# Kernel optimization log

Hardware: AMD Instinct MI355X
Metric: run time of the kernel (lower is better)

## Reference

```python
import jax
import jax.numpy as jnp
import numpy as np

NV, NH, COND_DIM, HW = 256, 256, 16, 64
B = 8192
T_END = 1.0
T_START = 5.0
FALLOFF = 0.1


def setup_inputs() -> dict:
    key = jax.random.key(0)
    ks = jax.random.split(key, 4)
    return {
        "cond": jax.random.normal(ks[0], (B, COND_DIM), dtype=jnp.float32),
        "W": jax.random.normal(ks[1], (NV, NH), dtype=jnp.float32) * 0.01,
        "b": jnp.zeros((NV,), jnp.float32),
        "c": jnp.zeros((NH,), jnp.float32),
        "fc1_w": jax.random.normal(ks[2], (HW, COND_DIM), dtype=jnp.float32) * (1.0 / np.sqrt(COND_DIM)),
        "fc1_b": jnp.zeros((HW,), jnp.float32),
        "fc2_w": jax.random.normal(ks[3], (2 * (NV + NH), HW), dtype=jnp.float32) * (1.0 / np.sqrt(HW)),
        "fc2_b": jnp.zeros((2 * (NV + NH),), jnp.float32),
        "steps": 32,
    }


def reference(cond, W, b, c, fc1_w, fc1_b, fc2_w, fc2_b, steps):
    nv, nh = W.shape
    # Conditioner: torch Linear convention y = x @ W.T + b
    x = jnp.tanh(cond @ fc1_w.T + fc1_b)
    x = x @ fc2_w.T + fc2_b  # [B, 2*(nv+nh)]
    gamma_b, beta_b, gamma_c, beta_c = jnp.split(x, [nv, 2 * nv, 2 * nv + nh], axis=-1)
    b_mod = (1.0 + gamma_b) * b + beta_b  # [B, nv]
    c_mod = (1.0 + gamma_c) * c + beta_c  # [B, nh]

    batch = cond.shape[0]
    key = jax.random.key(42)
    key, k0 = jax.random.split(key)
    v = jax.random.bernoulli(k0, 0.5, (batch, nv)).astype(W.dtype)
    s0 = jnp.ones((batch, 1), W.dtype)

    # sigmoid annealing schedule
    t = jnp.arange(steps, dtype=W.dtype)
    s = 1.0 / (1.0 + jnp.exp(FALLOFF * (t - steps / 2.0)))
    temps = T_END + (T_START - T_END) * s  # [steps]

    bsum = jnp.sum(b_mod, axis=-1)  # [B], constant across steps

    def gibbs_step(carry, T):
        v, s0, key = carry
        key, kh, ks0, kv = jax.random.split(key, 4)
        # symmetric flip of visibles
        v_eff = s0 * v + (1.0 - s0) * (1.0 - v)
        p_h = jax.nn.sigmoid((v_eff @ W + c_mod) / T)
        h = jax.random.bernoulli(kh, p_h).astype(v.dtype)  # [B, nh]
        a = h @ W.T  # [B, nv]
        vb = jnp.sum(v * b_mod, axis=-1)
        va = jnp.sum(v * a, axis=-1)
        asum = jnp.sum(a, axis=-1)
        dE = -bsum - asum + 2.0 * vb + 2.0 * va  # [B]
        p_s0 = jax.nn.sigmoid(dE / T)
        s0 = jax.random.bernoulli(ks0, p_s0).astype(v.dtype)[:, None]  # [B,1]
        p_v = jax.nn.sigmoid((a + b_mod) / T)
        v_eff2 = jax.random.bernoulli(kv, p_v).astype(v.dtype)
        v_next = s0 * v_eff2 + (1.0 - s0) * (1.0 - v_eff2)
        return (v_next, s0, key), None

    (v, s0, key), _ = jax.lax.scan(gibbs_step, (v, s0, key), temps)
    return v, temps
```

## Files before the change

kernel.cpp:

```cpp
#include <hip/hip_runtime.h>
#include <math.h>

#pragma clang fp contract(off)

namespace {

constexpr int kSteps = 32;

constexpr size_t OFF_TEMPS = 0;
constexpr size_t OFF_KEYS  = 64;
constexpr size_t OFF_WP    = 512;
constexpr size_t OFF_WTP   = 66048;
constexpr size_t OFF_F2T   = 131584;
constexpr size_t OFF_X1    = 197120;
constexpr size_t OFF_BMOD  = 721408;
constexpr size_t OFF_CMOD  = 2818560;
constexpr size_t WS_FLOATS = 4915712;

__device__ __forceinline__ unsigned rotl32(unsigned v, int n) {
  return (v << n) | (v >> (32 - n));
}

__device__ __forceinline__ void tf_block(unsigned k0, unsigned k1,
                                         unsigned c0, unsigned c1,
                                         unsigned* o0, unsigned* o1) {
  unsigned k2 = k0 ^ k1 ^ 0x1BD11BDAu;
  unsigned x0 = c0 + k0;
  unsigned x1 = c1 + k1;
  x0 += x1; x1 = rotl32(x1, 13); x1 ^= x0;
  x0 += x1; x1 = rotl32(x1, 15); x1 ^= x0;
  x0 += x1; x1 = rotl32(x1, 26); x1 ^= x0;
  x0 += x1; x1 = rotl32(x1, 6);  x1 ^= x0;
  x0 += k1; x1 += k2 + 1u;
  x0 += x1; x1 = rotl32(x1, 17); x1 ^= x0;
  x0 += x1; x1 = rotl32(x1, 29); x1 ^= x0;
  x0 += x1; x1 = rotl32(x1, 16); x1 ^= x0;
  x0 += x1; x1 = rotl32(x1, 24); x1 ^= x0;
  x0 += k2; x1 += k0 + 2u;
  x0 += x1; x1 = rotl32(x1, 13); x1 ^= x0;
  x0 += x1; x1 = rotl32(x1, 15); x1 ^= x0;
  x0 += x1; x1 = rotl32(x1, 26); x1 ^= x0;
  x0 += x1; x1 = rotl32(x1, 6);  x1 ^= x0;
  x0 += k0; x1 += k1 + 3u;
  x0 += x1; x1 = rotl32(x1, 17); x1 ^= x0;
  x0 += x1; x1 = rotl32(x1, 29); x1 ^= x0;
  x0 += x1; x1 = rotl32(x1, 16); x1 ^= x0;
  x0 += x1; x1 = rotl32(x1, 24); x1 ^= x0;
  x0 += k1; x1 += k2 + 4u;
  x0 += x1; x1 = rotl32(x1, 13); x1 ^= x0;
  x0 += x1; x1 = rotl32(x1, 15); x1 ^= x0;
  x0 += x1; x1 = rotl32(x1, 26); x1 ^= x0;
  x0 += x1; x1 = rotl32(x1, 6);  x1 ^= x0;
  x0 += k2; x1 += k0 + 5u;
  *o0 = x0; *o1 = x1;
}

__device__ __forceinline__ float tf_uniform(unsigned k0, unsigned k1, unsigned idx) {
  unsigned o0, o1;
  tf_block(k0, k1, 0u, idx, &o0, &o1);
  unsigned bits = o0 ^ o1;
  float f = __uint_as_float((bits >> 9) | 0x3f800000u);
  return f - 1.0f;
}

__device__ __forceinline__ float xla_tanhf(float x) {
  if (fabsf(x) < 0.0004f) return x;
  float xc = fminf(fmaxf(x, -9.0f), 9.0f);
  float x2 = xc * xc;
  float num = -2.76076847742355e-16f;
  num = num * x2 + 2.00018790482477e-13f;
  num = num * x2 + -8.60467152213735e-11f;
  num = num * x2 + 5.12229709037114e-08f;
  num = num * x2 + 1.48572235717979e-05f;
  num = num * x2 + 6.37261928875436e-04f;
  num = num * x2 + 4.89352455891786e-03f;
  num = xc * num;
  float den = 1.19825839466702e-06f;
  den = den * x2 + 1.18534705686654e-04f;
  den = den * x2 + 2.26843463243900e-03f;
  den = den * x2 + 4.89352518554385e-03f;
  return num / den;
}

__device__ __forceinline__ float xla_sigmoid(float x) {
  return 0.5f + 0.5f * xla_tanhf(0.5f * x);
}

__global__ __launch_bounds__(64) void kInitMeta(float* temps, unsigned* keys) {
  int t = threadIdx.x;
  if (t < 32) {
    float tf = (float)t;
    float arg = 0.1f * (tf - 16.0f);
    float e = (float)exp((double)arg);
    float s = 1.0f / (1.0f + e);
    temps[t] = 1.0f + 4.0f * s;
  }
  if (t == 0) {
    unsigned cur0 = 0u, cur1 = 42u;
    unsigned a0, a1, b0, b1;
    tf_block(cur0, cur1, 0u, 0u, &a0, &a1);
    tf_block(cur0, cur1, 0u, 1u, &b0, &b1);
    keys[0] = b0; keys[1] = b1;
    cur0 = a0; cur1 = a1;
    for (int st = 0; st < kSteps; ++st) {
      unsigned n0, n1, kh0, kh1, ks0a, ks0b, kv0, kv1;
      tf_block(cur0, cur1, 0u, 0u, &n0, &n1);
      tf_block(cur0, cur1, 0u, 1u, &kh0, &kh1);
      tf_block(cur0, cur1, 0u, 2u, &ks0a, &ks0b);
      tf_block(cur0, cur1, 0u, 3u, &kv0, &kv1);
      keys[2 + st * 6 + 0] = kh0;  keys[2 + st * 6 + 1] = kh1;
      keys[2 + st * 6 + 2] = ks0a; keys[2 + st * 6 + 3] = ks0b;
      keys[2 + st * 6 + 4] = kv0;  keys[2 + st * 6 + 5] = kv1;
      cur0 = n0; cur1 = n1;
    }
  }
}

__global__ __launch_bounds__(256) void kWp(const float* __restrict__ W, float4* __restrict__ Wp) {
  int idx = blockIdx.x * 256 + threadIdx.x;
  int kb = idx >> 8, j = idx & 255;
  float4 w;
  w.x = W[(4 * kb + 0) * 256 + j];
  w.y = W[(4 * kb + 1) * 256 + j];
  w.z = W[(4 * kb + 2) * 256 + j];
  w.w = W[(4 * kb + 3) * 256 + j];
  Wp[idx] = w;
}

__global__ __launch_bounds__(256) void kWtp(const float* __restrict__ W, float4* __restrict__ Wtp) {
  int idx = blockIdx.x * 256 + threadIdx.x;
  int kb = idx >> 8, i = idx & 255;
  float4 w;
  w.x = W[i * 256 + 4 * kb + 0];
  w.y = W[i * 256 + 4 * kb + 1];
  w.z = W[i * 256 + 4 * kb + 2];
  w.w = W[i * 256 + 4 * kb + 3];
  Wtp[idx] = w;
}

__global__ __launch_bounds__(256) void kTf2(const float* __restrict__ fc2w, float* __restrict__ fc2wT) {
  int idx = blockIdx.x * 256 + threadIdx.x;
  int k = idx >> 10, o = idx & 1023;
  fc2wT[idx] = fc2w[o * 64 + k];
}

__global__ __launch_bounds__(256) void kX1(const float* __restrict__ cond,
                                           const float* __restrict__ fc1w,
                                           const float* __restrict__ fc1b,
                                           float* __restrict__ x1) {
  int idx = blockIdx.x * 256 + threadIdx.x;
  int b = idx >> 6, hh = idx & 63;
  float acc = 0.0f;
  for (int k = 0; k < 16; ++k)
    acc = acc + cond[b * 16 + k] * fc1w[hh * 16 + k];
  acc = acc + fc1b[hh];
  x1[idx] = xla_tanhf(acc);
}

__global__ __launch_bounds__(256) void kMod2(const float* __restrict__ x1,
                                             const float* __restrict__ fc2wT,
                                             const float* __restrict__ fc2b,
                                             const float* __restrict__ bvec,
                                             const float* __restrict__ cvec,
                                             float* __restrict__ bmod,
                                             float* __restrict__ cmod) {
  const int bid = blockIdx.x;
  const int b = bid >> 1;
  const int half = bid & 1;
  const int ii = threadIdx.x;
  const int og = half * 512 + ii;
  const int ob = og + 256;
  float dg = 0.0f, db = 0.0f;
  for (int k = 0; k < 64; ++k) {
    float xv = x1[b * 64 + k];
    dg = dg + xv * fc2wT[k * 1024 + og];
    db = db + xv * fc2wT[k * 1024 + ob];
  }
  dg = dg + fc2b[og];
  db = db + fc2b[ob];
  float base = half ? cvec[ii] : bvec[ii];
  float outv = (1.0f + dg) * base + db;
  if (half) cmod[b * 256 + ii] = outv;
  else      bmod[b * 256 + ii] = outv;
}

__global__ __launch_bounds__(256, 4) void kGibbs(
    const float4* __restrict__ Wp, const float4* __restrict__ Wtp,
    const float* __restrict__ bmod, const float* __restrict__ cmod,
    const unsigned* __restrict__ keys, const float* __restrict__ temps,
    float* __restrict__ out) {
  __shared__ float4 X4[8][65];
  __shared__ float  vlds[8][257];
  __shared__ float  bmlds[8][257];
  __shared__ float  cmlds[8][257];
  __shared__ float  chainres[8][3];
  __shared__ float  bsum_s[8];
  __shared__ int    s0i[8];

  float* Xf = reinterpret_cast<float*>(X4);

  const int j = threadIdx.x;
  const int brow = blockIdx.x * 8;

#pragma unroll
  for (int r = 0; r < 8; ++r) {
    bmlds[r][j] = bmod[(brow + r) * 256 + j];
    cmlds[r][j] = cmod[(brow + r) * 256 + j];
  }
  if (j < 8) s0i[j] = 1;
  {
    const unsigned k00 = keys[0], k01 = keys[1];
#pragma unroll
    for (int r = 0; r < 8; ++r) {
      float u = tf_uniform(k00, k01, (unsigned)((brow + r) * 256 + j));
      vlds[r][j] = (u < 0.5f) ? 1.0f : 0.0f;
    }
  }
  __syncthreads();
  if (j < 8) {
    float s = 0.0f;
    for (int k = 0; k < 256; ++k) s = s + bmlds[j][k];
    bsum_s[j] = s;
  }

  for (int t = 0; t < kSteps; ++t) {
    const float T = temps[t];
    const unsigned kh0 = keys[2 + t * 6 + 0], kh1 = keys[2 + t * 6 + 1];
    const unsigned ksa = keys[2 + t * 6 + 2], ksb = keys[2 + t * 6 + 3];
    const unsigned kv0 = keys[2 + t * 6 + 4], kv1 = keys[2 + t * 6 + 5];

#pragma unroll
    for (int r = 0; r < 8; ++r) {
      float vv = vlds[r][j];
      Xf[r * 260 + j] = s0i[r] ? vv : 1.0f - vv;
    }
    __syncthreads();

    float acc[8];
#pragma unroll
    for (int r = 0; r < 8; ++r) acc[r] = 0.0f;
    {
      const float4* wp = Wp + j;
      for (int kb = 0; kb < 64; ++kb) {
        float4 w4 = wp[kb << 8];
#pragma unroll
        for (int r = 0; r < 8; ++r) {
          float4 v4 = X4[r][kb];
          acc[r] = __builtin_fmaf(v4.x, w4.x, acc[r]);
          acc[r] = __builtin_fmaf(v4.y, w4.y, acc[r]);
          acc[r] = __builtin_fmaf(v4.z, w4.z, acc[r]);
          acc[r] = __builtin_fmaf(v4.w, w4.w, acc[r]);
        }
      }
    }

    float hv[8];
#pragma unroll
    for (int r = 0; r < 8; ++r) {
      float z = (acc[r] + cmlds[r][j]) / T;
      float p = xla_sigmoid(z);
      float u = tf_uniform(kh0, kh1, (unsigned)((brow + r) * 256 + j));
      hv[r] = (u < p) ? 1.0f : 0.0f;
    }
    __syncthreads();
#pragma unroll
    for (int r = 0; r < 8; ++r) Xf[r * 260 + j] = hv[r];
    __syncthreads();

#pragma unroll
    for (int r = 0; r < 8; ++r) acc[r] = 0.0f;
    {
      const float4* wp = Wtp + j;
      for (int kb = 0; kb < 64; ++kb) {
        float4 w4 = wp[kb << 8];
#pragma unroll
        for (int r = 0; r < 8; ++r) {
          float4 v4 = X4[r][kb];
          acc[r] = __builtin_fmaf(v4.x, w4.x, acc[r]);
          acc[r] = __builtin_fmaf(v4.y, w4.y, acc[r]);
          acc[r] = __builtin_fmaf(v4.z, w4.z, acc[r]);
          acc[r] = __builtin_fmaf(v4.w, w4.w, acc[r]);
        }
      }
    }

    float ve2[8];
#pragma unroll
    for (int r = 0; r < 8; ++r) {
      float z = (acc[r] + bmlds[r][j]) / T;
      float p = xla_sigmoid(z);
      float u = tf_uniform(kv0, kv1, (unsigned)((brow + r) * 256 + j));
      ve2[r] = (u < p) ? 1.0f : 0.0f;
    }

    __syncthreads();
#pragma unroll
    for (int r = 0; r < 8; ++r) Xf[r * 260 + j] = acc[r];
    __syncthreads();

    if (j < 64) {
      if (j < 24) {
        const int r = j / 3, c = j % 3;
        const float* A = &vlds[r][0];
        const float* Y = (c == 0) ? &bmlds[r][0] : &Xf[r * 260];
        float s = 0.0f;
        for (int k = 0; k < 256; ++k) {
          float xm = (c == 2) ? 1.0f : A[k];
          s = __builtin_fmaf(xm, Y[k], s);
        }
        chainres[r][c] = s;
      }
    }
    __syncthreads();

    if (j < 8) {
      const int r = j;
      float vb = chainres[r][0], va = chainres[r][1], as = chainres[r][2];
      float dE = ((-bsum_s[r] - as) + 2.0f * vb) + 2.0f * va;
      float z = dE / T;
      float p = xla_sigmoid(z);
      float u = tf_uniform(ksa, ksb, (unsigned)(brow + r));
      s0i[r] = (u < p) ? 1 : 0;
    }
    __syncthreads();

#pragma unroll
    for (int r = 0; r < 8; ++r) {
      vlds[r][j] = s0i[r] ? ve2[r] : 1.0f - ve2[r];
    }
    __syncthreads();
  }

#pragma unroll
  for (int r = 0; r < 8; ++r)
    out[(brow + r) * 256 + j] = vlds[r][j];
  if (blockIdx.x == 0 && j < 32) out[2097152 + j] = temps[j];
}

}

extern "C" void kernel_launch(void* const* d_in, const int* in_sizes, int n_in,
                              void* d_out, int out_size, void* d_ws, size_t ws_size,
                              hipStream_t stream) {
  (void)in_sizes; (void)n_in; (void)out_size;
  const float* cond = (const float*)d_in[0];
  const float* W    = (const float*)d_in[1];
  const float* bvec = (const float*)d_in[2];
  const float* cvec = (const float*)d_in[3];
  const float* fc1w = (const float*)d_in[4];
  const float* fc1b = (const float*)d_in[5];
  const float* fc2w = (const float*)d_in[6];
  const float* fc2b = (const float*)d_in[7];

  if (ws_size < WS_FLOATS * sizeof(float)) return;

  float* ws      = (float*)d_ws;
  float* temps   = ws + OFF_TEMPS;
  unsigned* keys = (unsigned*)(ws + OFF_KEYS);
  float4* Wp     = (float4*)(ws + OFF_WP);
  float4* Wtp    = (float4*)(ws + OFF_WTP);
  float* fc2wT   = ws + OFF_F2T;
  float* x1      = ws + OFF_X1;
  float* bmod    = ws + OFF_BMOD;
  float* cmod    = ws + OFF_CMOD;
  float* out     = (float*)d_out;

  hipLaunchKernelGGL(kInitMeta, dim3(1), dim3(64), 0, stream, temps, keys);
  hipLaunchKernelGGL(kWp, dim3(256), dim3(256), 0, stream, W, Wp);
  hipLaunchKernelGGL(kWtp, dim3(256), dim3(256), 0, stream, W, Wtp);
  hipLaunchKernelGGL(kTf2, dim3(256), dim3(256), 0, stream, fc2w, fc2wT);
  hipLaunchKernelGGL(kX1, dim3(2048), dim3(256), 0, stream, cond, fc1w, fc1b, x1);
  hipLaunchKernelGGL(kMod2, dim3(16384), dim3(256), 0, stream, x1, fc2wT, fc2b, bvec, cvec, bmod, cmod);
  hipLaunchKernelGGL(kGibbs, dim3(1024), dim3(256), 0, stream, Wp, Wtp, bmod, cmod, keys, temps, out);
}
```

Before: 1.930 ms.

## Restructure Gibbs kernel into single-wavefront blocks without barriers

The Gibbs sampler now runs one 64-lane wavefront per block, handling 4 chains with each lane computing 4 columns. This lets it drop every __syncthreads in the step loop and rely on wavefront lockstep for shared-memory hand-offs. bmod and cmod are kept in registers, and the per-chain dot products read LDS as float4. In exchange, each block reuses every W load across only 4 chains instead of 8, so weight traffic through the caches doubles. The code also assumes the compiler keeps LDS accesses ordered within a wave even though no barrier or fence enforces it.

```diff
diff --git a/kernel.cpp b/kernel.cpp
--- a/kernel.cpp
+++ b/kernel.cpp
@@ -184,43 +184,48 @@
   else      bmod[b * 256 + ii] = outv;
 }
 
-__global__ __launch_bounds__(256, 4) void kGibbs(
+__global__ __launch_bounds__(64, 4) void kGibbs(
     const float4* __restrict__ Wp, const float4* __restrict__ Wtp,
     const float* __restrict__ bmod, const float* __restrict__ cmod,
     const unsigned* __restrict__ keys, const float* __restrict__ temps,
     float* __restrict__ out) {
-  __shared__ float4 X4[8][65];
-  __shared__ float  vlds[8][257];
-  __shared__ float  bmlds[8][257];
-  __shared__ float  cmlds[8][257];
-  __shared__ float  chainres[8][3];
-  __shared__ float  bsum_s[8];
-  __shared__ int    s0i[8];
-
-  float* Xf = reinterpret_cast<float*>(X4);
-
-  const int j = threadIdx.x;
-  const int brow = blockIdx.x * 8;
-
-#pragma unroll
-  for (int r = 0; r < 8; ++r) {
-    bmlds[r][j] = bmod[(brow + r) * 256 + j];
-    cmlds[r][j] = cmod[(brow + r) * 256 + j];
-  }
-  if (j < 8) s0i[j] = 1;
+  __shared__ float4 X4[4][65];
+  __shared__ float4 V4[4][65];
+  __shared__ float4 BM4[4][65];
+  __shared__ float  chainres[12];
+  __shared__ float  bsum_s[4];
+  __shared__ int    s0arr[4];
+
+  float* Xf  = reinterpret_cast<float*>(X4);
+  float* Vf  = reinterpret_cast<float*>(V4);
+  float* BMf = reinterpret_cast<float*>(BM4);
+
+  const int j0 = threadIdx.x;
+  const int brow = blockIdx.x * 4;
+
+  float cmv[4][4], bmv[4][4];
   {
     const unsigned k00 = keys[0], k01 = keys[1];
 #pragma unroll
-    for (int r = 0; r < 8; ++r) {
-      float u = tf_uniform(k00, k01, (unsigned)((brow + r) * 256 + j));
-      vlds[r][j] = (u < 0.5f) ? 1.0f : 0.0f;
-    }
-  }
-  __syncthreads();
-  if (j < 8) {
+    for (int r = 0; r < 4; ++r)
+#pragma unroll
+      for (int c = 0; c < 4; ++c) {
+        const int j = j0 + 64 * c;
+        const int gi = (brow + r) * 256 + j;
+        float bm = bmod[gi], cm = cmod[gi];
+        bmv[r][c] = bm; cmv[r][c] = cm;
+        BMf[r * 260 + j] = bm;
+        float u = tf_uniform(k00, k01, (unsigned)gi);
+        float vv = (u < 0.5f) ? 1.0f : 0.0f;
+        Vf[r * 260 + j] = vv;
+        Xf[r * 260 + j] = vv;
+      }
+  }
+  if (j0 < 4) {
+    const float* B = BMf + j0 * 260;
     float s = 0.0f;
-    for (int k = 0; k < 256; ++k) s = s + bmlds[j][k];
-    bsum_s[j] = s;
+    for (int k = 0; k < 256; ++k) s = s + B[k];
+    bsum_s[j0] = s;
   }
 
   for (int t = 0; t < kSteps; ++t) {
@@ -229,112 +234,148 @@
     const unsigned ksa = keys[2 + t * 6 + 2], ksb = keys[2 + t * 6 + 3];
     const unsigned kv0 = keys[2 + t * 6 + 4], kv1 = keys[2 + t * 6 + 5];
 
-#pragma unroll
-    for (int r = 0; r < 8; ++r) {
-      float vv = vlds[r][j];
-      Xf[r * 260 + j] = s0i[r] ? vv : 1.0f - vv;
-    }
-    __syncthreads();
-
-    float acc[8];
-#pragma unroll
-    for (int r = 0; r < 8; ++r) acc[r] = 0.0f;
-    {
-      const float4* wp = Wp + j;
-      for (int kb = 0; kb < 64; ++kb) {
-        float4 w4 = wp[kb << 8];
-#pragma unroll
-        for (int r = 0; r < 8; ++r) {
-          float4 v4 = X4[r][kb];
-          acc[r] = __builtin_fmaf(v4.x, w4.x, acc[r]);
-          acc[r] = __builtin_fmaf(v4.y, w4.y, acc[r]);
-          acc[r] = __builtin_fmaf(v4.z, w4.z, acc[r]);
-          acc[r] = __builtin_fmaf(v4.w, w4.w, acc[r]);
-        }
-      }
-    }
-
-    float hv[8];
-#pragma unroll
-    for (int r = 0; r < 8; ++r) {
-      float z = (acc[r] + cmlds[r][j]) / T;
-      float p = xla_sigmoid(z);
-      float u = tf_uniform(kh0, kh1, (unsigned)((brow + r) * 256 + j));
-      hv[r] = (u < p) ? 1.0f : 0.0f;
-    }
-    __syncthreads();
-#pragma unroll
-    for (int r = 0; r < 8; ++r) Xf[r * 260 + j] = hv[r];
-    __syncthreads();
-
-#pragma unroll
-    for (int r = 0; r < 8; ++r) acc[r] = 0.0f;
-    {
-      const float4* wp = Wtp + j;
-      for (int kb = 0; kb < 64; ++kb) {
-        float4 w4 = wp[kb << 8];
-#pragma unroll
-        for (int r = 0; r < 8; ++r) {
-          float4 v4 = X4[r][kb];
-          acc[r] = __builtin_fmaf(v4.x, w4.x, acc[r]);
-          acc[r] = __builtin_fmaf(v4.y, w4.y, acc[r]);
-          acc[r] = __builtin_fmaf(v4.z, w4.z, acc[r]);
-          acc[r] = __builtin_fmaf(v4.w, w4.w, acc[r]);
-        }
-      }
-    }
-
-    float ve2[8];
-#pragma unroll
-    for (int r = 0; r < 8; ++r) {
-      float z = (acc[r] + bmlds[r][j]) / T;
-      float p = xla_sigmoid(z);
-      float u = tf_uniform(kv0, kv1, (unsigned)((brow + r) * 256 + j));
-      ve2[r] = (u < p) ? 1.0f : 0.0f;
-    }
-
-    __syncthreads();
-#pragma unroll
-    for (int r = 0; r < 8; ++r) Xf[r * 260 + j] = acc[r];
-    __syncthreads();
-
-    if (j < 64) {
-      if (j < 24) {
-        const int r = j / 3, c = j % 3;
-        const float* A = &vlds[r][0];
-        const float* Y = (c == 0) ? &bmlds[r][0] : &Xf[r * 260];
-        float s = 0.0f;
-        for (int k = 0; k < 256; ++k) {
-          float xm = (c == 2) ? 1.0f : A[k];
-          s = __builtin_fmaf(xm, Y[k], s);
-        }
-        chainres[r][c] = s;
-      }
-    }
-    __syncthreads();
-
-    if (j < 8) {
-      const int r = j;
-      float vb = chainres[r][0], va = chainres[r][1], as = chainres[r][2];
+    float acc[4][4];
+
+#pragma unroll
+    for (int r = 0; r < 4; ++r)
+#pragma unroll
+      for (int c = 0; c < 4; ++c) acc[r][c] = 0.0f;
+    for (int kb = 0; kb < 64; ++kb) {
+      float4 w0 = Wp[(kb << 8) + j0];
+      float4 w1 = Wp[(kb << 8) + j0 + 64];
+      float4 w2 = Wp[(kb << 8) + j0 + 128];
+      float4 w3 = Wp[(kb << 8) + j0 + 192];
+#pragma unroll
+      for (int r = 0; r < 4; ++r) {
+        float4 x = X4[r][kb];
+        acc[r][0] = __builtin_fmaf(x.x, w0.x, acc[r][0]);
+        acc[r][0] = __builtin_fmaf(x.y, w0.y, acc[r][0]);
+        acc[r][0] = __builtin_fmaf(x.z, w0.z, acc[r][0]);
+        acc[r][0] = __builtin_fmaf(x.w, w0.w, acc[r][0]);
+        acc[r][1] = __builtin_fmaf(x.x, w1.x, acc[r][1]);
+        acc[r][1] = __builtin_fmaf(x.y, w1.y, acc[r][1]);
+        acc[r][1] = __builtin_fmaf(x.z, w1.z, acc[r][1]);
+        acc[r][1] = __builtin_fmaf(x.w, w1.w, acc[r][1]);
+        acc[r][2] = __builtin_fmaf(x.x, w2.x, acc[r][2]);
+        acc[r][2] = __builtin_fmaf(x.y, w2.y, acc[r][2]);
+        acc[r][2] = __builtin_fmaf(x.z, w2.z, acc[r][2]);
+        acc[r][2] = __builtin_fmaf(x.w, w2.w, acc[r][2]);
+        acc[r][3] = __builtin_fmaf(x.x, w3.x, acc[r][3]);
+        acc[r][3] = __builtin_fmaf(x.y, w3.y, acc[r][3]);
+        acc[r][3] = __builtin_fmaf(x.z, w3.z, acc[r][3]);
+        acc[r][3] = __builtin_fmaf(x.w, w3.w, acc[r][3]);
+      }
+    }
+
+#pragma unroll
+    for (int r = 0; r < 4; ++r)
+#pragma unroll
+      for (int c = 0; c < 4; ++c) {
+        const int j = j0 + 64 * c;
+        float z = (acc[r][c] + cmv[r][c]) / T;
+        float p = xla_sigmoid(z);
+        float u = tf_uniform(kh0, kh1, (unsigned)((brow + r) * 256 + j));
+        Xf[r * 260 + j] = (u < p) ? 1.0f : 0.0f;
+      }
+
+#pragma unroll
+    for (int r = 0; r < 4; ++r)
+#pragma unroll
+      for (int c = 0; c < 4; ++c) acc[r][c] = 0.0f;
+    for (int kb = 0; kb < 64; ++kb) {
+      float4 w0 = Wtp[(kb << 8) + j0];
+      float4 w1 = Wtp[(kb << 8) + j0 + 64];
+      float4 w2 = Wtp[(kb << 8) + j0 + 128];
+      float4 w3 = Wtp[(kb << 8) + j0 + 192];
+#pragma unroll
+      for (int r = 0; r < 4; ++r) {
+        float4 x = X4[r][kb];
+        acc[r][0] = __builtin_fmaf(x.x, w0.x, acc[r][0]);
+        acc[r][0] = __builtin_fmaf(x.y, w0.y, acc[r][0]);
+        acc[r][0] = __builtin_fmaf(x.z, w0.z, acc[r][0]);
+        acc[r][0] = __builtin_fmaf(x.w, w0.w, acc[r][0]);
+        acc[r][1] = __builtin_fmaf(x.x, w1.x, acc[r][1]);
+        acc[r][1] = __builtin_fmaf(x.y, w1.y, acc[r][1]);
+        acc[r][1] = __builtin_fmaf(x.z, w1.z, acc[r][1]);
+        acc[r][1] = __builtin_fmaf(x.w, w1.w, acc[r][1]);
+        acc[r][2] = __builtin_fmaf(x.x, w2.x, acc[r][2]);
+        acc[r][2] = __builtin_fmaf(x.y, w2.y, acc[r][2]);
+        acc[r][2] = __builtin_fmaf(x.z, w2.z, acc[r][2]);
+        acc[r][2] = __builtin_fmaf(x.w, w2.w, acc[r][2]);
+        acc[r][3] = __builtin_fmaf(x.x, w3.x, acc[r][3]);
+        acc[r][3] = __builtin_fmaf(x.y, w3.y, acc[r][3]);
+        acc[r][3] = __builtin_fmaf(x.z, w3.z, acc[r][3]);
+        acc[r][3] = __builtin_fmaf(x.w, w3.w, acc[r][3]);
+      }
+    }
+
+#pragma unroll
+    for (int r = 0; r < 4; ++r)
+#pragma unroll
+      for (int c = 0; c < 4; ++c)
+        Xf[r * 260 + j0 + 64 * c] = acc[r][c];
+
+    float ve2[4][4];
+#pragma unroll
+    for (int r = 0; r < 4; ++r)
+#pragma unroll
+      for (int c = 0; c < 4; ++c) {
+        const int j = j0 + 64 * c;
+        float z = (acc[r][c] + bmv[r][c]) / T;
+        float p = xla_sigmoid(z);
+        float u = tf_uniform(kv0, kv1, (unsigned)((brow + r) * 256 + j));
+        ve2[r][c] = (u < p) ? 1.0f : 0.0f;
+      }
+
+    if (j0 < 12) {
+      const int r = j0 / 3, c = j0 % 3;
+      const float4* A4 = reinterpret_cast<const float4*>(Vf + r * 260);
+      const float4* Y4 = reinterpret_cast<const float4*>(
+          ((c == 0) ? BMf : Xf) + r * 260);
+      const bool isAs = (c == 2);
+      float s = 0.0f;
+      for (int q = 0; q < 64; ++q) {
+        float4 a4 = A4[q];
+        float4 y4 = Y4[q];
+        float m0 = isAs ? 1.0f : a4.x; s = __builtin_fmaf(m0, y4.x, s);
+        float m1 = isAs ? 1.0f : a4.y; s = __builtin_fmaf(m1, y4.y, s);
+        float m2 = isAs ? 1.0f : a4.z; s = __builtin_fmaf(m2, y4.z, s);
+        float m3 = isAs ? 1.0f : a4.w; s = __builtin_fmaf(m3, y4.w, s);
+      }
+      chainres[j0] = s;
+    }
+
+    if (j0 < 4) {
+      const int r = j0;
+      float vb = chainres[3 * r], va = chainres[3 * r + 1], as = chainres[3 * r + 2];
       float dE = ((-bsum_s[r] - as) + 2.0f * vb) + 2.0f * va;
       float z = dE / T;
       float p = xla_sigmoid(z);
       float u = tf_uniform(ksa, ksb, (unsigned)(brow + r));
-      s0i[r] = (u < p) ? 1 : 0;
-    }
-    __syncthreads();
-
-#pragma unroll
-    for (int r = 0; r < 8; ++r) {
-      vlds[r][j] = s0i[r] ? ve2[r] : 1.0f - ve2[r];
-    }
-    __syncthreads();
-  }
-
-#pragma unroll
-  for (int r = 0; r < 8; ++r)
-    out[(brow + r) * 256 + j] = vlds[r][j];
-  if (blockIdx.x == 0 && j < 32) out[2097152 + j] = temps[j];
+      s0arr[r] = (u < p) ? 1 : 0;
+    }
+
+    int s0r0 = s0arr[0], s0r1 = s0arr[1], s0r2 = s0arr[2], s0r3 = s0arr[3];
+    int s0r[4] = {s0r0, s0r1, s0r2, s0r3};
+#pragma unroll
+    for (int r = 0; r < 4; ++r)
+#pragma unroll
+      for (int c = 0; c < 4; ++c) {
+        const int j = j0 + 64 * c;
+        float e = ve2[r][c];
+        Vf[r * 260 + j] = s0r[r] ? e : 1.0f - e;
+        Xf[r * 260 + j] = e;
+      }
+  }
+
+#pragma unroll
+  for (int r = 0; r < 4; ++r)
+#pragma unroll
+    for (int c = 0; c < 4; ++c) {
+      const int j = j0 + 64 * c;
+      out[(brow + r) * 256 + j] = Vf[r * 260 + j];
+    }
+  if (blockIdx.x == 0 && j0 < 32) out[2097152 + j0] = temps[j0];
 }
 
 }
@@ -371,5 +412,5 @@
   hipLaunchKernelGGL(kTf2, dim3(256), dim3(256), 0, stream, fc2w, fc2wT);
   hipLaunchKernelGGL(kX1, dim3(2048), dim3(256), 0, stream, cond, fc1w, fc1b, x1);
   hipLaunchKernelGGL(kMod2, dim3(16384), dim3(256), 0, stream, x1, fc2wT, fc2b, bvec, cvec, bmod, cmod);
-  hipLaunchKernelGGL(kGibbs, dim3(1024), dim3(256), 0, stream, Wp, Wtp, bmod, cmod, keys, temps, out);
-}
+  hipLaunchKernelGGL(kGibbs, dim3(2048), dim3(64), 0, stream, Wp, Wtp, bmod, cmod, keys, temps, out);
+}
```

New measurement: 2.721 ms. +41.0%, slower.

## Restructure Gibbs kernel to 4 chains per 128-thread block, two columns per thread

Applied to the files above, without the earlier changes.

The Gibbs kernel now processes 4 chains per block with 128 threads, each thread handling two hidden/visible columns, and launches twice as many blocks. bmod/cmod are kept in registers, and the per-chain energy reductions use float4 LDS reads over 12 threads instead of scalar reads over 24. This is meant to spread work over more blocks for better CU coverage and to cut LDS footprint and reduction latency. In exchange, each weight element is reused across only 4 chains per load instead of 8, which doubles global/L2 weight traffic per chain.

```diff
diff --git a/kernel.cpp b/kernel.cpp
--- a/kernel.cpp
+++ b/kernel.cpp
@@ -184,43 +184,51 @@
   else      bmod[b * 256 + ii] = outv;
 }
 
-__global__ __launch_bounds__(256, 4) void kGibbs(
+__global__ __launch_bounds__(128, 4) void kGibbs(
     const float4* __restrict__ Wp, const float4* __restrict__ Wtp,
     const float* __restrict__ bmod, const float* __restrict__ cmod,
     const unsigned* __restrict__ keys, const float* __restrict__ temps,
     float* __restrict__ out) {
-  __shared__ float4 X4[8][65];
-  __shared__ float  vlds[8][257];
-  __shared__ float  bmlds[8][257];
-  __shared__ float  cmlds[8][257];
-  __shared__ float  chainres[8][3];
-  __shared__ float  bsum_s[8];
-  __shared__ int    s0i[8];
-
-  float* Xf = reinterpret_cast<float*>(X4);
-
-  const int j = threadIdx.x;
-  const int brow = blockIdx.x * 8;
-
-#pragma unroll
-  for (int r = 0; r < 8; ++r) {
-    bmlds[r][j] = bmod[(brow + r) * 256 + j];
-    cmlds[r][j] = cmod[(brow + r) * 256 + j];
-  }
-  if (j < 8) s0i[j] = 1;
+  __shared__ float4 X4[4][65];
+  __shared__ float4 V4[4][65];
+  __shared__ float4 BM4[4][65];
+  __shared__ float  chainres[12];
+  __shared__ float  bsum_s[4];
+  __shared__ int    s0i[4];
+
+  float* Xf  = reinterpret_cast<float*>(X4);
+  float* Vf  = reinterpret_cast<float*>(V4);
+  float* BMf = reinterpret_cast<float*>(BM4);
+
+  const int j0 = threadIdx.x;
+  const int j1 = j0 + 128;
+  const int brow = blockIdx.x * 4;
+
+  float bmv[4][2], cmv[4][2];
   {
     const unsigned k00 = keys[0], k01 = keys[1];
 #pragma unroll
-    for (int r = 0; r < 8; ++r) {
-      float u = tf_uniform(k00, k01, (unsigned)((brow + r) * 256 + j));
-      vlds[r][j] = (u < 0.5f) ? 1.0f : 0.0f;
-    }
-  }
+    for (int r = 0; r < 4; ++r) {
+      const int g0 = (brow + r) * 256 + j0;
+      const int g1 = g0 + 128;
+      float bm0 = bmod[g0], bm1 = bmod[g1];
+      bmv[r][0] = bm0; bmv[r][1] = bm1;
+      cmv[r][0] = cmod[g0]; cmv[r][1] = cmod[g1];
+      BMf[r * 260 + j0] = bm0;
+      BMf[r * 260 + j1] = bm1;
+      float u0 = tf_uniform(k00, k01, (unsigned)g0);
+      float u1 = tf_uniform(k00, k01, (unsigned)g1);
+      Vf[r * 260 + j0] = (u0 < 0.5f) ? 1.0f : 0.0f;
+      Vf[r * 260 + j1] = (u1 < 0.5f) ? 1.0f : 0.0f;
+    }
+  }
+  if (j0 < 4) s0i[j0] = 1;
   __syncthreads();
-  if (j < 8) {
+  if (j0 < 4) {
+    const float* B = BMf + j0 * 260;
     float s = 0.0f;
-    for (int k = 0; k < 256; ++k) s = s + bmlds[j][k];
-    bsum_s[j] = s;
+    for (int k = 0; k < 256; ++k) s = s + B[k];
+    bsum_s[j0] = s;
   }
 
   for (int t = 0; t < kSteps; ++t) {
@@ -230,92 +238,126 @@
     const unsigned kv0 = keys[2 + t * 6 + 4], kv1 = keys[2 + t * 6 + 5];
 
 #pragma unroll
-    for (int r = 0; r < 8; ++r) {
-      float vv = vlds[r][j];
-      Xf[r * 260 + j] = s0i[r] ? vv : 1.0f - vv;
-    }
-    __syncthreads();
-
-    float acc[8];
-#pragma unroll
-    for (int r = 0; r < 8; ++r) acc[r] = 0.0f;
+    for (int r = 0; r < 4; ++r) {
+      float v0 = Vf[r * 260 + j0];
+      float v1 = Vf[r * 260 + j1];
+      Xf[r * 260 + j0] = s0i[r] ? v0 : 1.0f - v0;
+      Xf[r * 260 + j1] = s0i[r] ? v1 : 1.0f - v1;
+    }
+    __syncthreads();
+
+    float a0[4], a1[4];
+#pragma unroll
+    for (int r = 0; r < 4; ++r) { a0[r] = 0.0f; a1[r] = 0.0f; }
     {
-      const float4* wp = Wp + j;
+      const float4* wpa = Wp + j0;
+      const float4* wpb = Wp + j1;
       for (int kb = 0; kb < 64; ++kb) {
-        float4 w4 = wp[kb << 8];
-#pragma unroll
-        for (int r = 0; r < 8; ++r) {
-          float4 v4 = X4[r][kb];
-          acc[r] = __builtin_fmaf(v4.x, w4.x, acc[r]);
-          acc[r] = __builtin_fmaf(v4.y, w4.y, acc[r]);
-          acc[r] = __builtin_fmaf(v4.z, w4.z, acc[r]);
-          acc[r] = __builtin_fmaf(v4.w, w4.w, acc[r]);
+        float4 wa = wpa[kb << 8];
+        float4 wb = wpb[kb << 8];
+#pragma unroll
+        for (int r = 0; r < 4; ++r) {
+          float4 x = X4[r][kb];
+          a0[r] = __builtin_fmaf(x.x, wa.x, a0[r]);
+          a0[r] = __builtin_fmaf(x.y, wa.y, a0[r]);
+          a0[r] = __builtin_fmaf(x.z, wa.z, a0[r]);
+          a0[r] = __builtin_fmaf(x.w, wa.w, a0[r]);
+          a1[r] = __builtin_fmaf(x.x, wb.x, a1[r]);
+          a1[r] = __builtin_fmaf(x.y, wb.y, a1[r]);
+          a1[r] = __builtin_fmaf(x.z, wb.z, a1[r]);
+          a1[r] = __builtin_fmaf(x.w, wb.w, a1[r]);
         }
       }
     }
 
-    float hv[8];
-#pragma unroll
-    for (int r = 0; r < 8; ++r) {
-      float z = (acc[r] + cmlds[r][j]) / T;
-      float p = xla_sigmoid(z);
-      float u = tf_uniform(kh0, kh1, (unsigned)((brow + r) * 256 + j));
-      hv[r] = (u < p) ? 1.0f : 0.0f;
-    }
-    __syncthreads();
-#pragma unroll
-    for (int r = 0; r < 8; ++r) Xf[r * 260 + j] = hv[r];
-    __syncthreads();
-
-#pragma unroll
-    for (int r = 0; r < 8; ++r) acc[r] = 0.0f;
+    float hv0[4], hv1[4];
+#pragma unroll
+    for (int r = 0; r < 4; ++r) {
+      const int g0 = (brow + r) * 256 + j0;
+      float z0 = (a0[r] + cmv[r][0]) / T;
+      float p0 = xla_sigmoid(z0);
+      float u0 = tf_uniform(kh0, kh1, (unsigned)g0);
+      hv0[r] = (u0 < p0) ? 1.0f : 0.0f;
+      float z1 = (a1[r] + cmv[r][1]) / T;
+      float p1 = xla_sigmoid(z1);
+      float u1 = tf_uniform(kh0, kh1, (unsigned)(g0 + 128));
+      hv1[r] = (u1 < p1) ? 1.0f : 0.0f;
+    }
+    __syncthreads();
+#pragma unroll
+    for (int r = 0; r < 4; ++r) {
+      Xf[r * 260 + j0] = hv0[r];
+      Xf[r * 260 + j1] = hv1[r];
+    }
+    __syncthreads();
+
+#pragma unroll
+    for (int r = 0; r < 4; ++r) { a0[r] = 0.0f; a1[r] = 0.0f; }
     {
-      const float4* wp = Wtp + j;
+      const float4* wpa = Wtp + j0;
+      const float4* wpb = Wtp + j1;
       for (int kb = 0; kb < 64; ++kb) {
-        float4 w4 = wp[kb << 8];
-#pragma unroll
-        for (int r = 0; r < 8; ++r) {
-          float4 v4 = X4[r][kb];
-          acc[r] = __builtin_fmaf(v4.x, w4.x, acc[r]);
-          acc[r] = __builtin_fmaf(v4.y, w4.y, acc[r]);
-          acc[r] = __builtin_fmaf(v4.z, w4.z, acc[r]);
-          acc[r] = __builtin_fmaf(v4.w, w4.w, acc[r]);
+        float4 wa = wpa[kb << 8];
+        float4 wb = wpb[kb << 8];
+#pragma unroll
+        for (int r = 0; r < 4; ++r) {
+          float4 x = X4[r][kb];
+          a0[r] = __builtin_fmaf(x.x, wa.x, a0[r]);
+          a0[r] = __builtin_fmaf(x.y, wa.y, a0[r]);
+          a0[r] = __builtin_fmaf(x.z, wa.z, a0[r]);
+          a0[r] = __builtin_fmaf(x.w, wa.w, a0[r]);
+          a1[r] = __builtin_fmaf(x.x, wb.x, a1[r]);
+          a1[r] = __builtin_fmaf(x.y, wb.y, a1[r]);
+          a1[r] = __builtin_fmaf(x.z, wb.z, a1[r]);
+          a1[r] = __builtin_fmaf(x.w, wb.w, a1[r]);
         }
       }
     }
 
-    float ve2[8];
-#pragma unroll
-    for (int r = 0; r < 8; ++r) {
-      float z = (acc[r] + bmlds[r][j]) / T;
-      float p = xla_sigmoid(z);
-      float u = tf_uniform(kv0, kv1, (unsigned)((brow + r) * 256 + j));
-      ve2[r] = (u < p) ? 1.0f : 0.0f;
-    }
-
-    __syncthreads();
-#pragma unroll
-    for (int r = 0; r < 8; ++r) Xf[r * 260 + j] = acc[r];
-    __syncthreads();
-
-    if (j < 64) {
-      if (j < 24) {
-        const int r = j / 3, c = j % 3;
-        const float* A = &vlds[r][0];
-        const float* Y = (c == 0) ? &bmlds[r][0] : &Xf[r * 260];
-        float s = 0.0f;
-        for (int k = 0; k < 256; ++k) {
-          float xm = (c == 2) ? 1.0f : A[k];
-          s = __builtin_fmaf(xm, Y[k], s);
-        }
-        chainres[r][c] = s;
+    float ve20[4], ve21[4];
+#pragma unroll
+    for (int r = 0; r < 4; ++r) {
+      const int g0 = (brow + r) * 256 + j0;
+      float z0 = (a0[r] + bmv[r][0]) / T;
+      float p0 = xla_sigmoid(z0);
+      float u0 = tf_uniform(kv0, kv1, (unsigned)g0);
+      ve20[r] = (u0 < p0) ? 1.0f : 0.0f;
+      float z1 = (a1[r] + bmv[r][1]) / T;
+      float p1 = xla_sigmoid(z1);
+      float u1 = tf_uniform(kv0, kv1, (unsigned)(g0 + 128));
+      ve21[r] = (u1 < p1) ? 1.0f : 0.0f;
+    }
+
+    __syncthreads();
+#pragma unroll
+    for (int r = 0; r < 4; ++r) {
+      Xf[r * 260 + j0] = a0[r];
+      Xf[r * 260 + j1] = a1[r];
+    }
+    __syncthreads();
+
+    if (j0 < 12) {
+      const int r = j0 / 3, c = j0 % 3;
+      const float4* A4c = reinterpret_cast<const float4*>(Vf + r * 260);
+      const float4* Y4c = reinterpret_cast<const float4*>(
+          ((c == 0) ? BMf : Xf) + r * 260);
+      const bool isAs = (c == 2);
+      float s = 0.0f;
+      for (int q = 0; q < 64; ++q) {
+        float4 a4 = A4c[q];
+        float4 y4 = Y4c[q];
+        float m0 = isAs ? 1.0f : a4.x; s = __builtin_fmaf(m0, y4.x, s);
+        float m1 = isAs ? 1.0f : a4.y; s = __builtin_fmaf(m1, y4.y, s);
+        float m2 = isAs ? 1.0f : a4.z; s = __builtin_fmaf(m2, y4.z, s);
+        float m3 = isAs ? 1.0f : a4.w; s = __builtin_fmaf(m3, y4.w, s);
       }
-    }
-    __syncthreads();
-
-    if (j < 8) {
-      const int r = j;
-      float vb = chainres[r][0], va = chainres[r][1], as = chainres[r][2];
+      chainres[j0] = s;
+    }
+    __syncthreads();
+
+    if (j0 < 4) {
+      const int r = j0;
+      float vb = chainres[3 * r], va = chainres[3 * r + 1], as = chainres[3 * r + 2];
       float dE = ((-bsum_s[r] - as) + 2.0f * vb) + 2.0f * va;
       float z = dE / T;
       float p = xla_sigmoid(z);
@@ -325,16 +367,19 @@
     __syncthreads();
 
 #pragma unroll
-    for (int r = 0; r < 8; ++r) {
-      vlds[r][j] = s0i[r] ? ve2[r] : 1.0f - ve2[r];
-    }
-    __syncthreads();
-  }
-
-#pragma unroll
-  for (int r = 0; r < 8; ++r)
-    out[(brow + r) * 256 + j] = vlds[r][j];
-  if (blockIdx.x == 0 && j < 32) out[2097152 + j] = temps[j];
+    for (int r = 0; r < 4; ++r) {
+      Vf[r * 260 + j0] = s0i[r] ? ve20[r] : 1.0f - ve20[r];
+      Vf[r * 260 + j1] = s0i[r] ? ve21[r] : 1.0f - ve21[r];
+    }
+    __syncthreads();
+  }
+
+#pragma unroll
+  for (int r = 0; r < 4; ++r) {
+    out[(brow + r) * 256 + j0] = Vf[r * 260 + j0];
+    out[(brow + r) * 256 + j1] = Vf[r * 260 + j1];
+  }
+  if (blockIdx.x == 0 && j0 < 32) out[2097152 + j0] = temps[j0];
 }
 
 }
@@ -371,5 +416,5 @@
   hipLaunchKernelGGL(kTf2, dim3(256), dim3(256), 0, stream, fc2w, fc2wT);
   hipLaunchKernelGGL(kX1, dim3(2048), dim3(256), 0, stream, cond, fc1w, fc1b, x1);
   hipLaunchKernelGGL(kMod2, dim3(16384), dim3(256), 0, stream, x1, fc2wT, fc2b, bvec, cvec, bmod, cmod);
-  hipLaunchKernelGGL(kGibbs, dim3(1024), dim3(256), 0, stream, Wp, Wtp, bmod, cmod, keys, temps, out);
-}
+  hipLaunchKernelGGL(kGibbs, dim3(2048), dim3(128), 0, stream, Wp, Wtp, bmod, cmod, keys, temps, out);
+}
```

Result: faster. 1.796 ms (-6.9%).

## Process 16 chains per Gibbs block to halve weight reloads

Applied to the files above, without the earlier changes.

Each Gibbs block now handles 16 batch rows instead of 8, so every W and W^T float4 fetched from global/L2 is reused across twice as many chains. The grid is halved to 512 blocks. The kb loop is unrolled by 4 with loads hoisted, bmod/cmod are kept in registers, and the reduction phase uses float4 LDS reads across 48 threads. The cost is higher register pressure (launch bounds lowered to 2 waves) and only 512 blocks, which may underfill the 256 CUs and reduce latency hiding.

```diff
diff --git a/kernel.cpp b/kernel.cpp
--- a/kernel.cpp
+++ b/kernel.cpp
@@ -184,42 +184,44 @@
   else      bmod[b * 256 + ii] = outv;
 }
 
-__global__ __launch_bounds__(256, 4) void kGibbs(
+__global__ __launch_bounds__(256, 2) void kGibbs(
     const float4* __restrict__ Wp, const float4* __restrict__ Wtp,
     const float* __restrict__ bmod, const float* __restrict__ cmod,
     const unsigned* __restrict__ keys, const float* __restrict__ temps,
     float* __restrict__ out) {
-  __shared__ float4 X4[8][65];
-  __shared__ float  vlds[8][257];
-  __shared__ float  bmlds[8][257];
-  __shared__ float  cmlds[8][257];
-  __shared__ float  chainres[8][3];
-  __shared__ float  bsum_s[8];
-  __shared__ int    s0i[8];
-
-  float* Xf = reinterpret_cast<float*>(X4);
+  __shared__ float4 X4[16][65];
+  __shared__ float4 V4[16][65];
+  __shared__ float4 BM4[16][65];
+  __shared__ float  chainres[48];
+  __shared__ float  bsum_s[16];
+  __shared__ int    s0i[16];
+
+  float* Xf  = reinterpret_cast<float*>(X4);
+  float* Vf  = reinterpret_cast<float*>(V4);
+  float* BMf = reinterpret_cast<float*>(BM4);
 
   const int j = threadIdx.x;
-  const int brow = blockIdx.x * 8;
-
-#pragma unroll
-  for (int r = 0; r < 8; ++r) {
-    bmlds[r][j] = bmod[(brow + r) * 256 + j];
-    cmlds[r][j] = cmod[(brow + r) * 256 + j];
-  }
-  if (j < 8) s0i[j] = 1;
+  const int brow = blockIdx.x * 16;
+
+  float bmv[16], cmv[16];
   {
     const unsigned k00 = keys[0], k01 = keys[1];
 #pragma unroll
-    for (int r = 0; r < 8; ++r) {
-      float u = tf_uniform(k00, k01, (unsigned)((brow + r) * 256 + j));
-      vlds[r][j] = (u < 0.5f) ? 1.0f : 0.0f;
-    }
-  }
+    for (int r = 0; r < 16; ++r) {
+      const int gi = (brow + r) * 256 + j;
+      float bm = bmod[gi];
+      bmv[r] = bm; cmv[r] = cmod[gi];
+      BMf[r * 260 + j] = bm;
+      float u = tf_uniform(k00, k01, (unsigned)gi);
+      Vf[r * 260 + j] = (u < 0.5f) ? 1.0f : 0.0f;
+    }
+  }
+  if (j < 16) s0i[j] = 1;
   __syncthreads();
-  if (j < 8) {
+  if (j < 16) {
+    const float* B = BMf + j * 260;
     float s = 0.0f;
-    for (int k = 0; k < 256; ++k) s = s + bmlds[j][k];
+    for (int k = 0; k < 256; ++k) s = s + B[k];
     bsum_s[j] = s;
   }
 
@@ -230,64 +232,118 @@
     const unsigned kv0 = keys[2 + t * 6 + 4], kv1 = keys[2 + t * 6 + 5];
 
 #pragma unroll
-    for (int r = 0; r < 8; ++r) {
-      float vv = vlds[r][j];
+    for (int r = 0; r < 16; ++r) {
+      float vv = Vf[r * 260 + j];
       Xf[r * 260 + j] = s0i[r] ? vv : 1.0f - vv;
     }
     __syncthreads();
 
-    float acc[8];
-#pragma unroll
-    for (int r = 0; r < 8; ++r) acc[r] = 0.0f;
+    float acc[16];
+#pragma unroll
+    for (int r = 0; r < 16; ++r) acc[r] = 0.0f;
     {
       const float4* wp = Wp + j;
-      for (int kb = 0; kb < 64; ++kb) {
-        float4 w4 = wp[kb << 8];
-#pragma unroll
-        for (int r = 0; r < 8; ++r) {
-          float4 v4 = X4[r][kb];
-          acc[r] = __builtin_fmaf(v4.x, w4.x, acc[r]);
-          acc[r] = __builtin_fmaf(v4.y, w4.y, acc[r]);
-          acc[r] = __builtin_fmaf(v4.z, w4.z, acc[r]);
-          acc[r] = __builtin_fmaf(v4.w, w4.w, acc[r]);
+      for (int kb = 0; kb < 64; kb += 4) {
+        float4 wa = wp[(kb + 0) << 8];
+        float4 wb = wp[(kb + 1) << 8];
+        float4 wc = wp[(kb + 2) << 8];
+        float4 wd = wp[(kb + 3) << 8];
+#pragma unroll
+        for (int r = 0; r < 16; ++r) {
+          float4 x = X4[r][kb];
+          acc[r] = __builtin_fmaf(x.x, wa.x, acc[r]);
+          acc[r] = __builtin_fmaf(x.y, wa.y, acc[r]);
+          acc[r] = __builtin_fmaf(x.z, wa.z, acc[r]);
+          acc[r] = __builtin_fmaf(x.w, wa.w, acc[r]);
+        }
+#pragma unroll
+        for (int r = 0; r < 16; ++r) {
+          float4 x = X4[r][kb + 1];
+          acc[r] = __builtin_fmaf(x.x, wb.x, acc[r]);
+          acc[r] = __builtin_fmaf(x.y, wb.y, acc[r]);
+          acc[r] = __builtin_fmaf(x.z, wb.z, acc[r]);
+          acc[r] = __builtin_fmaf(x.w, wb.w, acc[r]);
+        }
+#pragma unroll
+        for (int r = 0; r < 16; ++r) {
+          float4 x = X4[r][kb + 2];
+          acc[r] = __builtin_fmaf(x.x, wc.x, acc[r]);
+          acc[r] = __builtin_fmaf(x.y, wc.y, acc[r]);
+          acc[r] = __builtin_fmaf(x.z, wc.z, acc[r]);
+          acc[r] = __builtin_fmaf(x.w, wc.w, acc[r]);
+        }
+#pragma unroll
+        for (int r = 0; r < 16; ++r) {
+          float4 x = X4[r][kb + 3];
+          acc[r] = __builtin_fmaf(x.x, wd.x, acc[r]);
+          acc[r] = __builtin_fmaf(x.y, wd.y, acc[r]);
+          acc[r] = __builtin_fmaf(x.z, wd.z, acc[r]);
+          acc[r] = __builtin_fmaf(x.w, wd.w, acc[r]);
         }
       }
     }
 
-    float hv[8];
-#pragma unroll
-    for (int r = 0; r < 8; ++r) {
-      float z = (acc[r] + cmlds[r][j]) / T;
+    float hv[16];
+#pragma unroll
+    for (int r = 0; r < 16; ++r) {
+      float z = (acc[r] + cmv[r]) / T;
       float p = xla_sigmoid(z);
       float u = tf_uniform(kh0, kh1, (unsigned)((brow + r) * 256 + j));
       hv[r] = (u < p) ? 1.0f : 0.0f;
     }
     __syncthreads();
 #pragma unroll
-    for (int r = 0; r < 8; ++r) Xf[r * 260 + j] = hv[r];
-    __syncthreads();
-
-#pragma unroll
-    for (int r = 0; r < 8; ++r) acc[r] = 0.0f;
+    for (int r = 0; r < 16; ++r) Xf[r * 260 + j] = hv[r];
+    __syncthreads();
+
+#pragma unroll
+    for (int r = 0; r < 16; ++r) acc[r] = 0.0f;
     {
       const float4* wp = Wtp + j;
-      for (int kb = 0; kb < 64; ++kb) {
-        float4 w4 = wp[kb << 8];
-#pragma unroll
-        for (int r = 0; r < 8; ++r) {
-          float4 v4 = X4[r][kb];
-          acc[r] = __builtin_fmaf(v4.x, w4.x, acc[r]);
-          acc[r] = __builtin_fmaf(v4.y, w4.y, acc[r]);
-          acc[r] = __builtin_fmaf(v4.z, w4.z, acc[r]);
-          acc[r] = __builtin_fmaf(v4.w, w4.w, acc[r]);
+      for (int kb = 0; kb < 64; kb += 4) {
+        float4 wa = wp[(kb + 0) << 8];
+        float4 wb = wp[(kb + 1) << 8];
+        float4 wc = wp[(kb + 2) << 8];
+        float4 wd = wp[(kb + 3) << 8];
+#pragma unroll
+        for (int r = 0; r < 16; ++r) {
+          float4 x = X4[r][kb];
+          acc[r] = __builtin_fmaf(x.x, wa.x, acc[r]);
+          acc[r] = __builtin_fmaf(x.y, wa.y, acc[r]);
+          acc[r] = __builtin_fmaf(x.z, wa.z, acc[r]);
+          acc[r] = __builtin_fmaf(x.w, wa.w, acc[r]);
+        }
+#pragma unroll
+        for (int r = 0; r < 16; ++r) {
+          float4 x = X4[r][kb + 1];
+          acc[r] = __builtin_fmaf(x.x, wb.x, acc[r]);
+          acc[r] = __builtin_fmaf(x.y, wb.y, acc[r]);
+          acc[r] = __builtin_fmaf(x.z, wb.z, acc[r]);
+          acc[r] = __builtin_fmaf(x.w, wb.w, acc[r]);
+        }
+#pragma unroll
+        for (int r = 0; r < 16; ++r) {
+          float4 x = X4[r][kb + 2];
+          acc[r] = __builtin_fmaf(x.x, wc.x, acc[r]);
+          acc[r] = __builtin_fmaf(x.y, wc.y, acc[r]);
+          acc[r] = __builtin_fmaf(x.z, wc.z, acc[r]);
+          acc[r] = __builtin_fmaf(x.w, wc.w, acc[r]);
+        }
+#pragma unroll
+        for (int r = 0; r < 16; ++r) {
+          float4 x = X4[r][kb + 3];
+          acc[r] = __builtin_fmaf(x.x, wd.x, acc[r]);
+          acc[r] = __builtin_fmaf(x.y, wd.y, acc[r]);
+          acc[r] = __builtin_fmaf(x.z, wd.z, acc[r]);
+          acc[r] = __builtin_fmaf(x.w, wd.w, acc[r]);
         }
       }
     }
 
-    float ve2[8];
-#pragma unroll
-    for (int r = 0; r < 8; ++r) {
-      float z = (acc[r] + bmlds[r][j]) / T;
+    float ve2[16];
+#pragma unroll
+    for (int r = 0; r < 16; ++r) {
+      float z = (acc[r] + bmv[r]) / T;
       float p = xla_sigmoid(z);
       float u = tf_uniform(kv0, kv1, (unsigned)((brow + r) * 256 + j));
       ve2[r] = (u < p) ? 1.0f : 0.0f;
@@ -295,27 +351,31 @@
 
     __syncthreads();
 #pragma unroll
-    for (int r = 0; r < 8; ++r) Xf[r * 260 + j] = acc[r];
-    __syncthreads();
-
-    if (j < 64) {
-      if (j < 24) {
-        const int r = j / 3, c = j % 3;
-        const float* A = &vlds[r][0];
-        const float* Y = (c == 0) ? &bmlds[r][0] : &Xf[r * 260];
-        float s = 0.0f;
-        for (int k = 0; k < 256; ++k) {
-          float xm = (c == 2) ? 1.0f : A[k];
-          s = __builtin_fmaf(xm, Y[k], s);
-        }
-        chainres[r][c] = s;
+    for (int r = 0; r < 16; ++r) Xf[r * 260 + j] = acc[r];
+    __syncthreads();
+
+    if (j < 48) {
+      const int r = j / 3, c = j % 3;
+      const float4* A4c = reinterpret_cast<const float4*>(Vf + r * 260);
+      const float4* Y4c = reinterpret_cast<const float4*>(
+          ((c == 0) ? BMf : Xf) + r * 260);
+      const bool isAs = (c == 2);
+      float s = 0.0f;
+      for (int q = 0; q < 64; ++q) {
+        float4 a4 = A4c[q];
+        float4 y4 = Y4c[q];
+        float m0 = isAs ? 1.0f : a4.x; s = __builtin_fmaf(m0, y4.x, s);
+        float m1 = isAs ? 1.0f : a4.y; s = __builtin_fmaf(m1, y4.y, s);
+        float m2 = isAs ? 1.0f : a4.z; s = __builtin_fmaf(m2, y4.z, s);
+        float m3 = isAs ? 1.0f : a4.w; s = __builtin_fmaf(m3, y4.w, s);
       }
-    }
-    __syncthreads();
-
-    if (j < 8) {
+      chainres[j] = s;
+    }
+    __syncthreads();
+
+    if (j < 16) {
       const int r = j;
-      float vb = chainres[r][0], va = chainres[r][1], as = chainres[r][2];
+      float vb = chainres[3 * r], va = chainres[3 * r + 1], as = chainres[3 * r + 2];
       float dE = ((-bsum_s[r] - as) + 2.0f * vb) + 2.0f * va;
       float z = dE / T;
       float p = xla_sigmoid(z);
@@ -325,15 +385,15 @@
     __syncthreads();
 
 #pragma unroll
-    for (int r = 0; r < 8; ++r) {
-      vlds[r][j] = s0i[r] ? ve2[r] : 1.0f - ve2[r];
-    }
-    __syncthreads();
-  }
-
-#pragma unroll
-  for (int r = 0; r < 8; ++r)
-    out[(brow + r) * 256 + j] = vlds[r][j];
+    for (int r = 0; r < 16; ++r) {
+      Vf[r * 260 + j] = s0i[r] ? ve2[r] : 1.0f - ve2[r];
+    }
+    __syncthreads();
+  }
+
+#pragma unroll
+  for (int r = 0; r < 16; ++r)
+    out[(brow + r) * 256 + j] = Vf[r * 260 + j];
   if (blockIdx.x == 0 && j < 32) out[2097152 + j] = temps[j];
 }
 
@@ -371,5 +431,5 @@
   hipLaunchKernelGGL(kTf2, dim3(256), dim3(256), 0, stream, fc2w, fc2wT);
   hipLaunchKernelGGL(kX1, dim3(2048), dim3(256), 0, stream, cond, fc1w, fc1b, x1);
   hipLaunchKernelGGL(kMod2, dim3(16384), dim3(256), 0, stream, x1, fc2wT, fc2b, bvec, cvec, bmod, cmod);
-  hipLaunchKernelGGL(kGibbs, dim3(1024), dim3(256), 0, stream, Wp, Wtp, bmod, cmod, keys, temps, out);
-}
+  hipLaunchKernelGGL(kGibbs, dim3(512), dim3(256), 0, stream, Wp, Wtp, bmod, cmod, keys, temps, out);
+}
```

After: 3.041 ms. 57.6% more time.
